# Performance work log

Measured on AMD Instinct MI355X. Metric: run time of the kernel, lower is better.

## Reference

```python
import jax, jax.numpy as jnp
import numpy as np

NUM_STATES = 16
INPUT_DIM = 1024
QUANTUM_DIM = 1024
LN_EPS = 1e-5


def setup_inputs() -> dict:
    key = jax.random.key(0)
    ks = jax.random.split(key, 7)
    # stacked per-state Linear weights: [S, input_dim, quantum_dim]
    W = jax.random.normal(ks[0], (NUM_STATES, INPUT_DIM, QUANTUM_DIM), jnp.float32) * (1.0 / np.sqrt(INPUT_DIM))
    b = jax.random.normal(ks[1], (NUM_STATES, QUANTUM_DIM), jnp.float32) * 0.01
    amplitude_weights = jax.random.normal(ks[2], (NUM_STATES, QUANTUM_DIM), jnp.float32)
    phase_weights = jax.random.normal(ks[3], (NUM_STATES, QUANTUM_DIM), jnp.float32)
    ln_gamma = jnp.ones((QUANTUM_DIM,), jnp.float32)
    ln_beta = jnp.zeros((QUANTUM_DIM,), jnp.float32)
    language_features = jax.random.normal(ks[4], (4096, INPUT_DIM), jnp.float32)
    return {
        "language_features": language_features,
        "W": W,
        "b": b,
        "amplitude_weights": amplitude_weights,
        "phase_weights": phase_weights,
        "ln_gamma": ln_gamma,
        "ln_beta": ln_beta,
    }


def reference(language_features, W, b, amplitude_weights, phase_weights, ln_gamma, ln_beta):
    # Per-state linear projections as one batched GEMM: [B, S, Q]
    states = jnp.einsum("bi,siq->bsq", language_features, W) + b[None, :, :]
    # amplitudes = softmax over states (dim=0 in torch)
    amplitudes = jax.nn.softmax(amplitude_weights, axis=0)  # [S, Q]
    # real(amplitude * exp(i*phase) * state) = amplitude * cos(phase) * state
    mix = amplitudes * jnp.cos(phase_weights)  # [S, Q]
    sup = states * mix[None, :, :]  # [B, S, Q]
    # LayerNorm over last dim
    mean = jnp.mean(sup, axis=-1, keepdims=True)
    var = jnp.var(sup, axis=-1, keepdims=True)
    out = (sup - mean) * jax.lax.rsqrt(var + LN_EPS) * ln_gamma + ln_beta
    return out
```

## Files before the change

kernel.cpp:

```cpp
#include <hip/hip_runtime.h>

typedef __attribute__((ext_vector_type(8))) short short8;
typedef __attribute__((ext_vector_type(4))) float f32x4;
typedef __attribute__((ext_vector_type(4))) unsigned short u16x4;

#define GLOAD16(g, l)                                                          \
  __builtin_amdgcn_global_load_lds(                                            \
      (const __attribute__((address_space(1))) unsigned int*)(g),              \
      (__attribute__((address_space(3))) unsigned int*)(l), 16, 0, 0)

__device__ __forceinline__ unsigned short f2bf(float f) {
  unsigned int u = __float_as_uint(f);
  u += 0x7FFFu + ((u >> 16) & 1u);
  return (unsigned short)(u >> 16);
}
__device__ __forceinline__ float bf2f(unsigned short h) {
  return __uint_as_float(((unsigned int)h) << 16);
}

__global__ void mix_kernel(const float* __restrict__ amp,
                           const float* __restrict__ phase,
                           const float* __restrict__ bias,
                           float* __restrict__ mix, float* __restrict__ bmix) {
  int q = blockIdx.x * blockDim.x + threadIdx.x;
  float a[16];
  float mx = -1e30f;
  for (int s = 0; s < 16; ++s) {
    a[s] = amp[s * 1024 + q];
    mx = fmaxf(mx, a[s]);
  }
  float sum = 0.f;
  for (int s = 0; s < 16; ++s) {
    a[s] = __expf(a[s] - mx);
    sum += a[s];
  }
  float inv = 1.f / sum;
  for (int s = 0; s < 16; ++s) {
    float m = a[s] * inv * cosf(phase[s * 1024 + q]);
    mix[s * 1024 + q] = m;
    bmix[s * 1024 + q] = bias[s * 1024 + q] * m;
  }
}

__global__ void cast_x_kernel(const float* __restrict__ x,
                              unsigned short* __restrict__ xb) {
  int i = (blockIdx.x * blockDim.x + threadIdx.x) * 4;
  float4 v = *(const float4*)(x + i);
  union { unsigned short h[4]; uint2 u; } o;
  o.h[0] = f2bf(v.x); o.h[1] = f2bf(v.y); o.h[2] = f2bf(v.z); o.h[3] = f2bf(v.w);
  *(uint2*)(xb + i) = o.u;
}

__global__ __launch_bounds__(256) void transpose_w_kernel(
    const float* __restrict__ W, const float* __restrict__ mix,
    unsigned short* __restrict__ Wt) {
  __shared__ unsigned short tile[64][68];
  const int s = blockIdx.z;
  const int q0 = blockIdx.x * 64, i0 = blockIdx.y * 64;
  const int t = threadIdx.x;
  const float* Ws = W + (size_t)s * 1048576;
  unsigned short* Wts = Wt + (size_t)s * 1048576;
  const int rq = (t & 15) * 4;
  const int ri = t >> 4;
  const float4 mv = *(const float4*)(mix + s * 1024 + q0 + rq);
  #pragma unroll
  for (int p = 0; p < 4; ++p) {
    const int i = p * 16 + ri;
    float4 v = *(const float4*)(Ws + (size_t)(i0 + i) * 1024 + q0 + rq);
    union { unsigned short h[4]; uint2 u; } pk;
    pk.h[0] = f2bf(v.x * mv.x);
    pk.h[1] = f2bf(v.y * mv.y);
    pk.h[2] = f2bf(v.z * mv.z);
    pk.h[3] = f2bf(v.w * mv.w);
    *(uint2*)&tile[i][rq] = pk.u;
  }
  __syncthreads();
  const int wq = t >> 2;
  const int wi = (t & 3) * 16;
  union { unsigned short h[8]; short8 v8; } u0, u1;
  #pragma unroll
  for (int e = 0; e < 8; ++e) {
    u0.h[e] = tile[wi + e][wq];
    u1.h[e] = tile[wi + 8 + e][wq];
  }
  unsigned short* dst = Wts + (size_t)(q0 + wq) * 1024 + i0 + wi;
  *(short8*)dst = u0.v8;
  *(short8*)(dst + 8) = u1.v8;
}

template <bool BF16SUP>
__global__ __launch_bounds__(256) void gemm_kernel(
    const unsigned short* __restrict__ xb, const unsigned short* __restrict__ wt,
    const float* __restrict__ bmix,
    float* __restrict__ outf, unsigned short* __restrict__ sup) {
  __shared__ __align__(16) unsigned short Abuf[3][128 * 32];
  __shared__ __align__(16) unsigned short Bbuf[3][128 * 32];

  const int tid = threadIdx.x;
  const int lane = tid & 63;
  const int wv = tid >> 6;
  const int wm = wv >> 1, wn = wv & 1;
  const int m0 = blockIdx.y * 128;
  const int n0 = blockIdx.x * 128;

  const int c0 = tid, c1 = tid + 256;
  const int r0 = c0 >> 2, k80 = (c0 & 3) * 8;
  const int r1 = c1 >> 2, k81 = (c1 & 3) * 8;
  const unsigned short* ga0 = xb + (size_t)(m0 + r0) * 1024 + k80;
  const unsigned short* ga1 = xb + (size_t)(m0 + r1) * 1024 + k81;
  const unsigned short* gb0 = wt + (size_t)(n0 + r0) * 1024 + k80;
  const unsigned short* gb1 = wt + (size_t)(n0 + r1) * 1024 + k81;

#define STAGE(kt, b) do {                                                      \
    const int _ko = (kt) * 32;                                                 \
    GLOAD16(ga0 + _ko, &Abuf[b][c0 * 8]);                                      \
    GLOAD16(ga1 + _ko, &Abuf[b][c1 * 8]);                                      \
    GLOAD16(gb0 + _ko, &Bbuf[b][c0 * 8]);                                      \
    GLOAD16(gb1 + _ko, &Bbuf[b][c1 * 8]);                                      \
  } while (0)

  f32x4 acc[4][4];
  #pragma unroll
  for (int i = 0; i < 4; ++i)
    #pragma unroll
    for (int j = 0; j < 4; ++j) acc[i][j] = (f32x4){0.f, 0.f, 0.f, 0.f};

  const int lr = lane & 15;
  const int lk = (lane >> 4) * 8;

#define READS(AF, BF, b) do {                                                  \
    const unsigned short* _ab = &Abuf[b][(wm * 64 + lr) * 32 + lk];            \
    _Pragma("unroll")                                                          \
    for (int mi = 0; mi < 4; ++mi)                                             \
      AF[mi] = *(const short8*)(_ab + mi * 16 * 32);                           \
    const unsigned short* _bb = &Bbuf[b][(wn * 64 + lr) * 32 + lk];            \
    _Pragma("unroll")                                                          \
    for (int ni = 0; ni < 4; ++ni)                                             \
      BF[ni] = *(const short8*)(_bb + ni * 16 * 32);                           \
  } while (0)

#define MFMASET(AF, BF)                                                        \
    _Pragma("unroll")                                                          \
    for (int mi = 0; mi < 4; ++mi)                                             \
      _Pragma("unroll")                                                        \
      for (int ni = 0; ni < 4; ++ni)                                           \
        acc[mi][ni] = __builtin_amdgcn_mfma_f32_16x16x32_bf16(                 \
            AF[mi], BF[ni], acc[mi][ni], 0, 0, 0)

#define LGKM0() do { asm volatile("s_waitcnt lgkmcnt(0)" ::: "memory");        \
                     __builtin_amdgcn_sched_barrier(0); } while (0)

  short8 afA[4], bfA[4], afB[4], bfB[4];

  STAGE(0, 0);
  STAGE(1, 1);
  asm volatile("s_waitcnt vmcnt(4)" ::: "memory");
  __builtin_amdgcn_s_barrier();
  READS(afA, bfA, 0);

  int b0 = 0;
  #pragma unroll 1
  for (int it = 0; it < 16; ++it) {
    const int kt0 = 2 * it, kt1 = kt0 + 1;
    int b1 = b0 + 1; if (b1 >= 3) b1 -= 3;
    int b2 = b0 + 2; if (b2 >= 3) b2 -= 3;
    if (kt0 < 30) STAGE(kt0 + 2, b2);
    LGKM0();
    if (kt0 < 30) asm volatile("s_waitcnt vmcnt(4)" ::: "memory");
    else          asm volatile("s_waitcnt vmcnt(0)" ::: "memory");
    __builtin_amdgcn_sched_barrier(0);
    __builtin_amdgcn_s_barrier();
    READS(afB, bfB, b1);
    MFMASET(afA, bfA);
    if (kt1 < 30) STAGE(kt1 + 2, b0);
    LGKM0();
    if (kt1 < 30) asm volatile("s_waitcnt vmcnt(4)" ::: "memory");
    __builtin_amdgcn_sched_barrier(0);
    __builtin_amdgcn_s_barrier();
    if (kt1 < 31) READS(afA, bfA, b2);
    MFMASET(afB, bfB);
    b0 = b2;
  }
#undef STAGE
#undef READS
#undef MFMASET
#undef LGKM0

  #pragma unroll
  for (int ni = 0; ni < 4; ++ni) {
    const int n = n0 + wn * 64 + ni * 16 + lr;
    const float bv = bmix[n];
    #pragma unroll
    for (int mi = 0; mi < 4; ++mi) {
      const int m = m0 + wm * 64 + mi * 16 + (lane >> 4) * 4;
      #pragma unroll
      for (int r = 0; r < 4; ++r) {
        float v = acc[mi][ni][r] + bv;
        if (BF16SUP)
          sup[(size_t)(m + r) * 16384 + n] = f2bf(v);
        else
          outf[(size_t)(m + r) * 16384 + n] = v;
      }
    }
  }
}

__global__ __launch_bounds__(256) void ln_bf16_kernel(
    const unsigned short* __restrict__ sup, float* __restrict__ out,
    const float* __restrict__ gamma, const float* __restrict__ beta) {
  __shared__ float red[8];
  const int t = threadIdx.x;
  const size_t base = (size_t)blockIdx.x * 1024;
  u16x4 raw = *(const u16x4*)(sup + base + t * 4);
  float v[4];
  #pragma unroll
  for (int j = 0; j < 4; ++j) v[j] = bf2f(raw[j]);
  float s = v[0] + v[1] + v[2] + v[3];
  float ss = v[0] * v[0] + v[1] * v[1] + v[2] * v[2] + v[3] * v[3];
  #pragma unroll
  for (int m = 32; m >= 1; m >>= 1) {
    s += __shfl_xor(s, m);
    ss += __shfl_xor(ss, m);
  }
  const int wv = t >> 6;
  if ((t & 63) == 0) { red[wv * 2] = s; red[wv * 2 + 1] = ss; }
  __syncthreads();
  const float S = red[0] + red[2] + red[4] + red[6];
  const float SS = red[1] + red[3] + red[5] + red[7];
  const float mean = S * (1.0f / 1024.0f);
  const float var = SS * (1.0f / 1024.0f) - mean * mean;
  const float rstd = rsqrtf(var + 1e-5f);
  const float4 g = *(const float4*)(gamma + t * 4);
  const float4 b = *(const float4*)(beta + t * 4);
  float4 o;
  o.x = (v[0] - mean) * rstd * g.x + b.x;
  o.y = (v[1] - mean) * rstd * g.y + b.y;
  o.z = (v[2] - mean) * rstd * g.z + b.z;
  o.w = (v[3] - mean) * rstd * g.w + b.w;
  *(float4*)(out + base + t * 4) = o;
}

__global__ __launch_bounds__(256) void ln_kernel(float* __restrict__ out,
                                                 const float* __restrict__ gamma,
                                                 const float* __restrict__ beta) {
  __shared__ float red[8];
  const int t = threadIdx.x;
  const size_t base = (size_t)blockIdx.x * 1024;
  float4 v = *(const float4*)(out + base + t * 4);
  float s = v.x + v.y + v.z + v.w;
  float ss = v.x * v.x + v.y * v.y + v.z * v.z + v.w * v.w;
  #pragma unroll
  for (int m = 32; m >= 1; m >>= 1) {
    s += __shfl_xor(s, m);
    ss += __shfl_xor(ss, m);
  }
  const int wv = t >> 6;
  if ((t & 63) == 0) { red[wv * 2] = s; red[wv * 2 + 1] = ss; }
  __syncthreads();
  const float S = red[0] + red[2] + red[4] + red[6];
  const float SS = red[1] + red[3] + red[5] + red[7];
  const float mean = S * (1.0f / 1024.0f);
  const float var = SS * (1.0f / 1024.0f) - mean * mean;
  const float rstd = rsqrtf(var + 1e-5f);
  const float4 g = *(const float4*)(gamma + t * 4);
  const float4 b = *(const float4*)(beta + t * 4);
  float4 o;
  o.x = (v.x - mean) * rstd * g.x + b.x;
  o.y = (v.y - mean) * rstd * g.y + b.y;
  o.z = (v.z - mean) * rstd * g.z + b.z;
  o.w = (v.w - mean) * rstd * g.w + b.w;
  *(float4*)(out + base + t * 4) = o;
}

extern "C" void kernel_launch(void* const* d_in, const int* in_sizes, int n_in,
                              void* d_out, int out_size, void* d_ws, size_t ws_size,
                              hipStream_t stream) {
  (void)in_sizes; (void)n_in; (void)out_size;
  const float* x     = (const float*)d_in[0];
  const float* W     = (const float*)d_in[1];
  const float* bias  = (const float*)d_in[2];
  const float* amp   = (const float*)d_in[3];
  const float* phase = (const float*)d_in[4];
  const float* gamma = (const float*)d_in[5];
  const float* beta  = (const float*)d_in[6];
  float* out = (float*)d_out;

  const bool big = ws_size >= (size_t)134217728ULL;

  unsigned short *Wt, *xbuf, *supb = nullptr;
  float *mixp, *bmixp;
  if (big) {
    char* ob = (char*)d_out;
    Wt    = (unsigned short*)ob;
    xbuf  = (unsigned short*)(ob + 33554432);
    mixp  = (float*)(ob + 41943040);
    bmixp = mixp + 16384;
    supb  = (unsigned short*)d_ws;
  } else {
    char* ws = (char*)d_ws;
    Wt    = (unsigned short*)ws;
    xbuf  = (unsigned short*)(ws + 33554432);
    mixp  = (float*)(ws + 33554432 + 8388608);
    bmixp = mixp + 16384;
  }

  hipLaunchKernelGGL(mix_kernel, dim3(4), dim3(256), 0, stream, amp, phase, bias, mixp, bmixp);
  hipLaunchKernelGGL(cast_x_kernel, dim3(4096), dim3(256), 0, stream, x, xbuf);
  hipLaunchKernelGGL(transpose_w_kernel, dim3(16, 16, 16), dim3(256), 0, stream, W, mixp, Wt);
  if (big) {
    hipLaunchKernelGGL((gemm_kernel<true>), dim3(128, 32), dim3(256), 0, stream,
                       xbuf, Wt, bmixp, out, supb);
    hipLaunchKernelGGL(ln_bf16_kernel, dim3(65536), dim3(256), 0, stream,
                       supb, out, gamma, beta);
  } else {
    hipLaunchKernelGGL((gemm_kernel<false>), dim3(128, 32), dim3(256), 0, stream,
                       xbuf, Wt, bmixp, out, nullptr);
    hipLaunchKernelGGL(ln_kernel, dim3(65536), dim3(256), 0, stream, out, gamma, beta);
  }
}
```

Measured before the change: 299.6 us.

## Load GEMM A operand directly from global into registers, bypassing LDS

The A tile is no longer staged through shared memory. Each wave now loads its own MFMA A fragments straight from global memory into registers, double-buffered across even and odd k-steps, while B keeps the three-stage LDS pipeline. This halves LDS capacity and LDS read traffic and cuts the LDS writes for A. In exchange, A rows are fetched twice (once by each wn wave) with less coalesced 16-byte-per-lane loads. The tightened vmcnt(2) waits may also block on the A loads issued just before them, exposing global latency.

```diff
diff --git a/kernel.cpp b/kernel.cpp
--- a/kernel.cpp
+++ b/kernel.cpp
@@ -93,7 +93,6 @@
     const unsigned short* __restrict__ xb, const unsigned short* __restrict__ wt,
     const float* __restrict__ bmix,
     float* __restrict__ outf, unsigned short* __restrict__ sup) {
-  __shared__ __align__(16) unsigned short Abuf[3][128 * 32];
   __shared__ __align__(16) unsigned short Bbuf[3][128 * 32];
 
   const int tid = threadIdx.x;
@@ -103,36 +102,29 @@
   const int m0 = blockIdx.y * 128;
   const int n0 = blockIdx.x * 128;
 
+  const int lr = lane & 15;
+  const int lk = (lane >> 4) * 8;
+
   const int c0 = tid, c1 = tid + 256;
   const int r0 = c0 >> 2, k80 = (c0 & 3) * 8;
   const int r1 = c1 >> 2, k81 = (c1 & 3) * 8;
-  const unsigned short* ga0 = xb + (size_t)(m0 + r0) * 1024 + k80;
-  const unsigned short* ga1 = xb + (size_t)(m0 + r1) * 1024 + k81;
   const unsigned short* gb0 = wt + (size_t)(n0 + r0) * 1024 + k80;
   const unsigned short* gb1 = wt + (size_t)(n0 + r1) * 1024 + k81;
-
-#define STAGE(kt, b) do {                                                      \
+  const unsigned short* pA = xb + (size_t)(m0 + wm * 64 + lr) * 1024 + lk;
+
+#define SB(kt, b) do {                                                         \
     const int _ko = (kt) * 32;                                                 \
-    GLOAD16(ga0 + _ko, &Abuf[b][c0 * 8]);                                      \
-    GLOAD16(ga1 + _ko, &Abuf[b][c1 * 8]);                                      \
     GLOAD16(gb0 + _ko, &Bbuf[b][c0 * 8]);                                      \
     GLOAD16(gb1 + _ko, &Bbuf[b][c1 * 8]);                                      \
   } while (0)
 
-  f32x4 acc[4][4];
-  #pragma unroll
-  for (int i = 0; i < 4; ++i)
-    #pragma unroll
-    for (int j = 0; j < 4; ++j) acc[i][j] = (f32x4){0.f, 0.f, 0.f, 0.f};
-
-  const int lr = lane & 15;
-  const int lk = (lane >> 4) * 8;
-
-#define READS(AF, BF, b) do {                                                  \
-    const unsigned short* _ab = &Abuf[b][(wm * 64 + lr) * 32 + lk];            \
+#define LA(kt, DST) do {                                                       \
     _Pragma("unroll")                                                          \
     for (int mi = 0; mi < 4; ++mi)                                             \
-      AF[mi] = *(const short8*)(_ab + mi * 16 * 32);                           \
+      DST[mi] = *(const short8*)(pA + (size_t)mi * 16384 + (kt) * 32);         \
+  } while (0)
+
+#define RDB(BF, b) do {                                                        \
     const unsigned short* _bb = &Bbuf[b][(wn * 64 + lr) * 32 + lk];            \
     _Pragma("unroll")                                                          \
     for (int ni = 0; ni < 4; ++ni)                                             \
@@ -147,16 +139,20 @@
         acc[mi][ni] = __builtin_amdgcn_mfma_f32_16x16x32_bf16(                 \
             AF[mi], BF[ni], acc[mi][ni], 0, 0, 0)
 
-#define LGKM0() do { asm volatile("s_waitcnt lgkmcnt(0)" ::: "memory");        \
-                     __builtin_amdgcn_sched_barrier(0); } while (0)
-
-  short8 afA[4], bfA[4], afB[4], bfB[4];
-
-  STAGE(0, 0);
-  STAGE(1, 1);
+  f32x4 acc[4][4];
+  #pragma unroll
+  for (int i = 0; i < 4; ++i)
+    #pragma unroll
+    for (int j = 0; j < 4; ++j) acc[i][j] = (f32x4){0.f, 0.f, 0.f, 0.f};
+
+  short8 aE[4], aO[4], bq[4];
+
+  SB(0, 0);
+  SB(1, 1);
+  LA(0, aE);
+  LA(1, aO);
   asm volatile("s_waitcnt vmcnt(4)" ::: "memory");
   __builtin_amdgcn_s_barrier();
-  READS(afA, bfA, 0);
 
   int b0 = 0;
   #pragma unroll 1
@@ -164,27 +160,29 @@
     const int kt0 = 2 * it, kt1 = kt0 + 1;
     int b1 = b0 + 1; if (b1 >= 3) b1 -= 3;
     int b2 = b0 + 2; if (b2 >= 3) b2 -= 3;
-    if (kt0 < 30) STAGE(kt0 + 2, b2);
-    LGKM0();
-    if (kt0 < 30) asm volatile("s_waitcnt vmcnt(4)" ::: "memory");
+    RDB(bq, b0);
+    if (kt0 < 30) SB(kt0 + 2, b2);
+    asm volatile("s_waitcnt lgkmcnt(0)" ::: "memory");
+    if (kt0 < 30) asm volatile("s_waitcnt vmcnt(2)" ::: "memory");
     else          asm volatile("s_waitcnt vmcnt(0)" ::: "memory");
     __builtin_amdgcn_sched_barrier(0);
     __builtin_amdgcn_s_barrier();
-    READS(afB, bfB, b1);
-    MFMASET(afA, bfA);
-    if (kt1 < 30) STAGE(kt1 + 2, b0);
-    LGKM0();
-    if (kt1 < 30) asm volatile("s_waitcnt vmcnt(4)" ::: "memory");
+    MFMASET(aE, bq);
+    if (kt0 < 30) LA(kt0 + 2, aE);
+    RDB(bq, b1);
+    if (kt1 < 30) SB(kt1 + 2, b0);
+    asm volatile("s_waitcnt lgkmcnt(0)" ::: "memory");
+    if (kt1 < 30) asm volatile("s_waitcnt vmcnt(2)" ::: "memory");
     __builtin_amdgcn_sched_barrier(0);
     __builtin_amdgcn_s_barrier();
-    if (kt1 < 31) READS(afA, bfA, b2);
-    MFMASET(afB, bfB);
+    MFMASET(aO, bq);
+    if (kt1 < 30) LA(kt1 + 2, aO);
     b0 = b2;
   }
-#undef STAGE
-#undef READS
+#undef SB
+#undef LA
+#undef RDB
 #undef MFMASET
-#undef LGKM0
 
   #pragma unroll
   for (int ni = 0; ni < 4; ++ni) {
```

Result: slower. 414.9 us (+38.5%).
